# Kernel optimization log

Measured on AMD Instinct MI355X. Metric: run time of the kernel, lower is better.

The kernel has to match this reference:

```python
import jax, jax.numpy as jnp
import numpy as np

BN_EPS = 1e-5
NUM_BITS = 8          # activation quantization bits
NUM_BITS_WEIGHT = 8   # weight quantization bits


def _ste(x, q):
    # straight-through estimator: forward = q, backward = identity
    return x + jax.lax.stop_gradient(q - x)


def quant_signed(x, bits):
    # symmetric signed per-tensor uniform quantization (input_signed=True / weights with sign=True)
    qmax = float(2 ** (bits - 1) - 1)
    scale = jnp.max(jnp.abs(x)) / qmax + 1e-12
    q = jnp.clip(jnp.round(x / scale), -qmax - 1.0, qmax) * scale
    return _ste(x, q)


def quant_unsigned(x, bits):
    # unsigned per-tensor uniform quantization (input_signed=False, post-ReLU activations)
    qmax = float(2 ** bits - 1)
    scale = jnp.max(x) / qmax + 1e-12
    q = jnp.clip(jnp.round(x / scale), 0.0, qmax) * scale
    return _ste(x, q)


def conv3x3(x, w, stride=1):
    # x: [N,C,H,W], w: [O,I,3,3], padding=1, no bias
    return jax.lax.conv_general_dilated(
        x, w, window_strides=(stride, stride), padding=((1, 1), (1, 1)),
        dimension_numbers=('NCHW', 'OIHW', 'NCHW'))


def batchnorm(x, gamma, beta):
    # training-mode BN: per-batch statistics over (N,H,W)
    mean = jnp.mean(x, axis=(0, 2, 3), keepdims=True)
    var = jnp.var(x, axis=(0, 2, 3), keepdims=True)
    xn = (x - mean) * jax.lax.rsqrt(var + BN_EPS)
    return xn * gamma[None, :, None, None] + beta[None, :, None, None]


def setup_inputs() -> dict:
    key = jax.random.key(0)
    k1, k2, k3 = jax.random.split(key, 3)
    B, C, H, W = 64, 256, 32, 32
    x = jax.random.normal(k1, (B, C, H, W), dtype=jnp.float32)
    fan = C * 9
    w1 = jax.random.normal(k2, (C, C, 3, 3), dtype=jnp.float32) * np.sqrt(2.0 / fan)
    w2 = jax.random.normal(k3, (C, C, 3, 3), dtype=jnp.float32) * np.sqrt(2.0 / fan)
    gamma1 = jnp.ones((C,), jnp.float32)
    beta1 = jnp.zeros((C,), jnp.float32)
    gamma2 = jnp.ones((C,), jnp.float32)
    beta2 = jnp.zeros((C,), jnp.float32)
    return {'x': x, 'w1': w1, 'gamma1': gamma1, 'beta1': beta1,
            'w2': w2, 'gamma2': gamma2, 'beta2': beta2}


def reference(x, w1, gamma1, beta1, w2, gamma2, beta2):
    residual = x
    # conv1: input_signed=True -> signed 8-bit act quant; weight 8-bit signed quant
    qx = quant_signed(x, NUM_BITS)
    qw1 = quant_signed(w1, NUM_BITS_WEIGHT)
    out = conv3x3(qx, qw1, stride=1)
    out = batchnorm(out, gamma1, beta1)
    out = jax.nn.relu(out)
    # conv2: input_signed=False -> unsigned 8-bit act quant (post-ReLU)
    qo = quant_unsigned(out, NUM_BITS)
    qw2 = quant_signed(w2, NUM_BITS_WEIGHT)
    out = conv3x3(qo, qw2, stride=1)
    out = batchnorm(out, gamma2, beta2)
    out = out + residual
    out = jax.nn.relu(out)
    return out
```

## Files before the change

kernel.cpp:

```cpp
#include <hip/hip_runtime.h>

typedef unsigned short US;
typedef __attribute__((ext_vector_type(8))) short bf16x8;
typedef __attribute__((ext_vector_type(4))) float f32x4;

typedef __attribute__((address_space(1))) unsigned int uglobal;
typedef __attribute__((address_space(3))) unsigned int ulocal;

__device__ __forceinline__ void async16(const void* g, void* l) {
  __builtin_amdgcn_global_load_lds((const uglobal*)g, (ulocal*)l, 16, 0, 0);
}

__device__ __forceinline__ US f2bf(float f) {
  union { float f; unsigned u; } v; v.f = f;
  return (US)(v.u >> 16);
}

__device__ __forceinline__ float u2f(unsigned u) { return __uint_as_float(u); }

__global__ __launch_bounds__(256) void absmax3_kernel(const float* __restrict__ x,
                                                      const float* __restrict__ w1,
                                                      const float* __restrict__ w2,
                                                      unsigned* __restrict__ sc) {
  int b = blockIdx.x;
  const float* src; int n4, b0, nb, seg;
  if (b < 1792)      { src = x;  n4 = 4194304; b0 = 0;    nb = 1792; seg = 0; }
  else if (b < 1856) { src = w1; n4 = 147456;  b0 = 1792; nb = 64;   seg = 1; }
  else               { src = w2; n4 = 147456;  b0 = 1856; nb = 64;   seg = 2; }
  float m = 0.f;
  int stride = nb * 256;
  for (int i = (b - b0) * 256 + threadIdx.x; i < n4; i += stride) {
    float4 v = ((const float4*)src)[i];
    m = fmaxf(fmaxf(fabsf(v.x), fabsf(v.y)), fmaxf(fmaxf(fabsf(v.z), fabsf(v.w)), m));
  }
  for (int off = 32; off; off >>= 1) m = fmaxf(m, __shfl_down(m, off, 64));
  __shared__ float sm[4];
  int lane = threadIdx.x & 63, wv = threadIdx.x >> 6;
  if (!lane) sm[wv] = m;
  __syncthreads();
  if (threadIdx.x == 0)
    atomicMax(sc + seg, __float_as_uint(fmaxf(fmaxf(sm[0], sm[1]), fmaxf(sm[2], sm[3]))));
}

__global__ __launch_bounds__(256) void quantw_kernel(const float* __restrict__ w, US* __restrict__ wq,
                                                     const unsigned* __restrict__ sc, int sidx) {
  int j = blockIdx.x * 256 + threadIdx.x;
  if (j >= 256 * 2304) return;
  float s = u2f(sc[sidx]) / 127.f + 1e-12f;
  int o = j / 2304, k = j - o * 2304, khw = k >> 8, c = k & 255;
  float q = fminf(fmaxf(rintf(w[(size_t)(o * 256 + c) * 9 + khw] / s), -128.f), 127.f);
  wq[j] = f2bf(q);
}

__global__ __launch_bounds__(256) void quantx_kernel(const float* __restrict__ x,
                                                     US* __restrict__ halo,
                                                     const unsigned* __restrict__ sc) {
  int n = blockIdx.x >> 5, h = blockIdx.x & 31;
  float s = u2f(sc[0]) / 127.f + 1e-12f;
  __shared__ float lds[32 * 257];
  const float* src = x + (size_t)n * 256 * 1024 + h * 32;
  int t = threadIdx.x;
  int wloc = t & 31, crow = t >> 5;
  for (int cc = 0; cc < 256; cc += 8) {
    int c = cc + crow;
    lds[wloc * 257 + c] = src[(size_t)c * 1024 + wloc];
  }
  __syncthreads();
  US* dst = halo + ((size_t)((n * 34 + h + 1) * 34) + 1) * 256;
  for (int w_ = 0; w_ < 32; ++w_) {
    float v = lds[w_ * 257 + t];
    float q = fminf(fmaxf(rintf(v / s), -128.f), 127.f);
    dst[(size_t)w_ * 256 + t] = f2bf(q);
  }
}

template <int MODE>
__global__ __launch_bounds__(512) void conv8_kernel(const US* __restrict__ aptr,
                                                    const US* __restrict__ bptr,
                                                    float* __restrict__ out,
                                                    const unsigned* __restrict__ sc,
                                                    float* __restrict__ part) {
  extern __shared__ char smem[];
  const int tid = threadIdx.x, lane = tid & 63, wid = tid >> 6;
  const int wm = wid >> 2, wn = wid & 3;
  int bid = blockIdx.x;
  bid = (bid & 7) * 32 + (bid >> 3);
  const int pixBase = bid * 256;

  long gA[2], gB[2];
  int ldst[2];
#pragma unroll
  for (int j = 0; j < 2; ++j) {
    int d = tid * 16 + j * 8192;
    int rp = d >> 7, s = (d >> 4) & 7, sp = s ^ (rp & 7);
    int row = rp * 2 + (sp >> 2), kl = (sp & 3) * 8;
    ldst[j] = d;
    int p = pixBase + row;
    int n = p >> 10, h = (p >> 5) & 31, w_ = p & 31;
    long ghalo = (long)((n * 34 + h) * 34 + w_) * 512 + kl * 2;
    long gwt = (long)row * 4608 + kl * 2;
    if (MODE == 0) { gA[j] = ghalo; gB[j] = gwt; }
    else           { gA[j] = gwt;  gB[j] = ghalo; }
  }

  const int g = lane >> 4, l15 = lane & 15;
  int aOff[8], bOff[4];
#pragma unroll
  for (int m = 0; m < 8; ++m) {
    int row = wm * 128 + m * 16 + l15; int rp = row >> 1;
    aOff[m] = rp * 128 + ((((((row & 1) << 2) | g)) ^ (rp & 7)) << 4);
  }
#pragma unroll
  for (int n = 0; n < 4; ++n) {
    int row = wn * 64 + n * 16 + l15; int rp = row >> 1;
    bOff[n] = rp * 128 + ((((((row & 1) << 2) | g)) ^ (rp & 7)) << 4);
  }

  const char* ac = (const char*)aptr;
  const char* bc = (const char*)bptr;
  char* lds = smem;

  auto stage = [&](int P) {
    int cblk = P / 9, khw = P - cblk * 9;
    int kh = khw / 3, kw = khw - kh * 3;
    long uH = (long)(kh * 34 + kw) * 512 + cblk * 64;
    long uW = (long)khw * 512 + cblk * 64;
    long uA = (MODE == 0) ? uH : uW;
    long uB = (MODE == 0) ? uW : uH;
    char* rb = lds + (P & 3) * 32768;
    async16(ac + gA[0] + uA, rb + ldst[0]);
    async16(ac + gA[1] + uA, rb + ldst[1]);
    async16(bc + gB[0] + uB, rb + 16384 + ldst[0]);
    async16(bc + gB[1] + uB, rb + 16384 + ldst[1]);
  };

  f32x4 acc[8][4];
#pragma unroll
  for (int m = 0; m < 8; ++m)
#pragma unroll
    for (int n = 0; n < 4; ++n)
#pragma unroll
      for (int r = 0; r < 4; ++r) acc[m][n][r] = 0.f;

  stage(0); stage(1); stage(2);
  asm volatile("s_waitcnt vmcnt(8)" ::: "memory");
  asm volatile("s_barrier" ::: "memory");

  for (int P = 0; P < 72; ++P) {
    if (P < 69) stage(P + 3);
    const char* rb = lds + (P & 3) * 32768;
    bf16x8 a[8], b[4];
#pragma unroll
    for (int m = 0; m < 8; ++m) a[m] = *(const bf16x8*)(rb + aOff[m]);
#pragma unroll
    for (int n = 0; n < 4; ++n) b[n] = *(const bf16x8*)(rb + 16384 + bOff[n]);
    __builtin_amdgcn_s_setprio(1);
#pragma unroll
    for (int m = 0; m < 8; ++m)
#pragma unroll
      for (int n = 0; n < 4; ++n)
        acc[m][n] = __builtin_amdgcn_mfma_f32_16x16x32_bf16(a[m], b[n], acc[m][n], 0, 0, 0);
    __builtin_amdgcn_s_setprio(0);
    if (P < 69)      asm volatile("s_waitcnt vmcnt(8)" ::: "memory");
    else if (P == 69) asm volatile("s_waitcnt vmcnt(4)" ::: "memory");
    else if (P == 70) asm volatile("s_waitcnt vmcnt(0)" ::: "memory");
    if (P < 71) asm volatile("s_barrier" ::: "memory");
  }
  __syncthreads();

  if constexpr (MODE == 0) {
    const float s = (u2f(sc[0]) / 127.f + 1e-12f) * (u2f(sc[1]) / 127.f + 1e-12f);
    float vs[4], vss[4], vmx[4], vmn[4];
#pragma unroll
    for (int n = 0; n < 4; ++n) { vs[n] = 0.f; vss[n] = 0.f; vmx[n] = -3.4e38f; vmn[n] = 3.4e38f; }
#pragma unroll
    for (int m = 0; m < 8; ++m) {
      int p0 = pixBase + wm * 128 + m * 16 + g * 4;
#pragma unroll
      for (int n = 0; n < 4; ++n) {
        int ch = wn * 64 + n * 16 + l15;
#pragma unroll
        for (int r = 0; r < 4; ++r) {
          float v = acc[m][n][r] * s;
          out[(size_t)(p0 + r) * 256 + ch] = v;
          vs[n] += v; vss[n] += v * v;
          vmx[n] = fmaxf(vmx[n], v); vmn[n] = fminf(vmn[n], v);
        }
      }
    }
#pragma unroll
    for (int off = 16; off <= 32; off <<= 1)
#pragma unroll
      for (int n = 0; n < 4; ++n) {
        vs[n] += __shfl_xor(vs[n], off, 64);
        vss[n] += __shfl_xor(vss[n], off, 64);
        vmx[n] = fmaxf(vmx[n], __shfl_xor(vmx[n], off, 64));
        vmn[n] = fminf(vmn[n], __shfl_xor(vmn[n], off, 64));
      }
    float* S0 = (float*)smem;
    float* S1 = S0 + 512;
    float* S2 = S0 + 1024;
    float* S3 = S0 + 1536;
    if (lane < 16) {
#pragma unroll
      for (int n = 0; n < 4; ++n) {
        int ch = wn * 64 + n * 16 + l15;
        S0[wm * 256 + ch] = vs[n]; S1[wm * 256 + ch] = vss[n];
        S2[wm * 256 + ch] = vmx[n]; S3[wm * 256 + ch] = vmn[n];
      }
    }
    __syncthreads();
    if (tid < 256) {
      int idx = bid * 256 + tid;
      part[idx]          = S0[tid] + S0[256 + tid];
      part[65536 + idx]  = S1[tid] + S1[256 + tid];
      part[131072 + idx] = fmaxf(S2[tid], S2[256 + tid]);
      part[196608 + idx] = fminf(S3[tid], S3[256 + tid]);
    }
  } else {
    const float s = (u2f(sc[3]) / 255.f + 1e-12f) * (u2f(sc[2]) / 127.f + 1e-12f);
    float* SS = (float*)smem;
    float* SQ = SS + 1024;
#pragma unroll
    for (int m = 0; m < 8; ++m) {
      float sr[4], sq[4];
#pragma unroll
      for (int r = 0; r < 4; ++r) { sr[r] = 0.f; sq[r] = 0.f; }
      int o0 = wm * 128 + m * 16 + g * 4;
#pragma unroll
      for (int n = 0; n < 4; ++n) {
        int p = pixBase + wn * 64 + n * 16 + l15;
#pragma unroll
        for (int r = 0; r < 4; ++r) {
          float v = acc[m][n][r] * s;
          out[(size_t)(o0 + r) * 65536 + p] = v;
          sr[r] += v; sq[r] += v * v;
        }
      }
#pragma unroll
      for (int off = 1; off <= 8; off <<= 1)
#pragma unroll
        for (int r = 0; r < 4; ++r) {
          sr[r] += __shfl_xor(sr[r], off, 64);
          sq[r] += __shfl_xor(sq[r], off, 64);
        }
      if (l15 == 0) {
#pragma unroll
        for (int r = 0; r < 4; ++r) {
          SS[wn * 256 + o0 + r] = sr[r];
          SQ[wn * 256 + o0 + r] = sq[r];
        }
      }
    }
    __syncthreads();
    if (tid < 256) {
      float a = 0.f, b = 0.f;
#pragma unroll
      for (int w = 0; w < 4; ++w) { a += SS[w * 256 + tid]; b += SQ[w * 256 + tid]; }
      part[bid * 256 + tid] = a;
      part[65536 + bid * 256 + tid] = b;
    }
  }
}

__global__ __launch_bounds__(256) void bn1fin_kernel(const float* __restrict__ part,
                                                     const float* __restrict__ g,
                                                     const float* __restrict__ be,
                                                     float* __restrict__ bnA, float* __restrict__ bnB,
                                                     unsigned* __restrict__ sc) {
  int o0 = blockIdx.x * 32;
  int t = threadIdx.x, oc = t & 31, mq = t >> 5;
  float s = 0.f, ss = 0.f, mx = -3.4e38f, mn = 3.4e38f;
  for (int j = 0; j < 32; ++j) {
    int i = (mq * 32 + j) * 256 + o0 + oc;
    s += part[i]; ss += part[65536 + i];
    mx = fmaxf(mx, part[131072 + i]); mn = fminf(mn, part[196608 + i]);
  }
  __shared__ float red[4][8][32];
  red[0][mq][oc] = s; red[1][mq][oc] = ss; red[2][mq][oc] = mx; red[3][mq][oc] = mn;
  __syncthreads();
  if (t < 32) {
    s = 0.f; ss = 0.f; mx = -3.4e38f; mn = 3.4e38f;
    for (int q = 0; q < 8; ++q) {
      s += red[0][q][t]; ss += red[1][q][t];
      mx = fmaxf(mx, red[2][q][t]); mn = fminf(mn, red[3][q][t]);
    }
    float mean = s * (1.f / 65536.f);
    float var = fmaxf(ss * (1.f / 65536.f) - mean * mean, 0.f);
    int o = o0 + t;
    float a = g[o] * rsqrtf(var + 1e-5f);
    float b2 = be[o] - mean * a;
    bnA[o] = a; bnB[o] = b2;
    float m = fmaxf(fmaxf(a * mx + b2, a * mn + b2), 0.f);
    atomicMax(sc + 3, __float_as_uint(m));
  }
}

__global__ __launch_bounds__(256) void bn2fin_kernel(const float* __restrict__ part,
                                                     const float* __restrict__ g,
                                                     const float* __restrict__ be,
                                                     float* __restrict__ bnA2, float* __restrict__ bnB2) {
  int o0 = blockIdx.x * 32;
  int t = threadIdx.x, oc = t & 31, mq = t >> 5;
  float s = 0.f, ss = 0.f;
  for (int j = 0; j < 32; ++j) {
    int i = (mq * 32 + j) * 256 + o0 + oc;
    s += part[i]; ss += part[65536 + i];
  }
  __shared__ float red[2][8][32];
  red[0][mq][oc] = s; red[1][mq][oc] = ss;
  __syncthreads();
  if (t < 32) {
    s = 0.f; ss = 0.f;
    for (int q = 0; q < 8; ++q) { s += red[0][q][t]; ss += red[1][q][t]; }
    float mean = s * (1.f / 65536.f);
    float var = fmaxf(ss * (1.f / 65536.f) - mean * mean, 0.f);
    int o = o0 + t;
    float a = g[o] * rsqrtf(var + 1e-5f);
    bnA2[o] = a;
    bnB2[o] = be[o] - mean * a;
  }
}

__global__ __launch_bounds__(256) void apply_kernel(const float* __restrict__ y,
                                                    const float* __restrict__ bnA,
                                                    const float* __restrict__ bnB,
                                                    const unsigned* __restrict__ sc,
                                                    US* __restrict__ halo) {
  int t = threadIdx.x;
  int c4 = (t & 63) * 4;
  int psub = t >> 6;
  float s2 = u2f(sc[3]) / 255.f + 1e-12f;
  float4 a = *(const float4*)(bnA + c4);
  float4 b = *(const float4*)(bnB + c4);
  int p0 = blockIdx.x * 16 + psub;
  for (int j = 0; j < 4; ++j) {
    int p = p0 + j * 4;
    float4 v = *(const float4*)(y + (size_t)p * 256 + c4);
    ushort4 q;
    q.x = f2bf(fminf(fmaxf(rintf(fmaxf(a.x * v.x + b.x, 0.f) / s2), 0.f), 255.f));
    q.y = f2bf(fminf(fmaxf(rintf(fmaxf(a.y * v.y + b.y, 0.f) / s2), 0.f), 255.f));
    q.z = f2bf(fminf(fmaxf(rintf(fmaxf(a.z * v.z + b.z, 0.f) / s2), 0.f), 255.f));
    q.w = f2bf(fminf(fmaxf(rintf(fmaxf(a.w * v.w + b.w, 0.f) / s2), 0.f), 255.f));
    int n = p >> 10, h = (p >> 5) & 31, w_ = p & 31;
    *(ushort4*)(halo + ((size_t)((n * 34 + h + 1) * 34) + (w_ + 1)) * 256 + c4) = q;
  }
}

__global__ __launch_bounds__(256) void final_kernel(const float* __restrict__ y2,
                                                    const float* __restrict__ x,
                                                    const float* __restrict__ bnA2,
                                                    const float* __restrict__ bnB2,
                                                    float* __restrict__ out) {
  int tid = blockIdx.x * 256 + threadIdx.x;
  for (int i = tid; i < 4194304; i += 1048576) {
    int e = i << 2;
    int o = (e >> 10) & 255;
    int n = e >> 18, hw = e & 1023;
    float4 v = *(const float4*)(y2 + (((size_t)o << 16) + (n << 10) + hw));
    float4 xr = ((const float4*)x)[i];
    float a = bnA2[o], b = bnB2[o];
    float4 r;
    r.x = fmaxf(a * v.x + b + xr.x, 0.f);
    r.y = fmaxf(a * v.y + b + xr.y, 0.f);
    r.z = fmaxf(a * v.z + b + xr.z, 0.f);
    r.w = fmaxf(a * v.w + b + xr.w, 0.f);
    ((float4*)out)[i] = r;
  }
}

extern "C" void kernel_launch(void* const* d_in, const int* in_sizes, int n_in,
                              void* d_out, int out_size, void* d_ws, size_t ws_size,
                              hipStream_t stream) {
  const float* x  = (const float*)d_in[0];
  const float* w1 = (const float*)d_in[1];
  const float* g1 = (const float*)d_in[2];
  const float* b1 = (const float*)d_in[3];
  const float* w2 = (const float*)d_in[4];
  const float* g2 = (const float*)d_in[5];
  const float* b2 = (const float*)d_in[6];
  float* out = (float*)d_out;
  char* ws = (char*)d_ws;

  unsigned* sc = (unsigned*)ws;
  float* bnA   = (float*)(ws + 8192);
  float* bnB   = (float*)(ws + 12288);
  float* bnA2  = (float*)(ws + 16384);
  float* bnB2  = (float*)(ws + 20480);
  float* part  = (float*)(ws + 24576);
  US* wq1  = (US*)(ws + 24576 + 2097152);
  US* wq2  = (US*)(ws + 24576 + 2097152 + 1179648);
  US* halo = (US*)(ws + 24576 + 2097152 + 2 * 1179648);
  float* convb = (float*)(ws + 24576 + 2097152 + 2 * 1179648 + 37879808);

  hipFuncSetAttribute((const void*)(conv8_kernel<0>), hipFuncAttributeMaxDynamicSharedMemorySize, 131072);
  hipFuncSetAttribute((const void*)(conv8_kernel<1>), hipFuncAttributeMaxDynamicSharedMemorySize, 131072);

  hipMemsetAsync(sc, 0, 64, stream);
  hipMemsetAsync(halo, 0, 37879808, stream);

  absmax3_kernel<<<1920, 256, 0, stream>>>(x, w1, w2, sc);
  quantw_kernel<<<2304, 256, 0, stream>>>(w1, wq1, sc, 1);
  quantw_kernel<<<2304, 256, 0, stream>>>(w2, wq2, sc, 2);
  quantx_kernel<<<2048, 256, 0, stream>>>(x, halo, sc);
  conv8_kernel<0><<<256, 512, 131072, stream>>>(halo, wq1, convb, sc, part);
  bn1fin_kernel<<<8, 256, 0, stream>>>(part, g1, b1, bnA, bnB, sc);
  apply_kernel<<<4096, 256, 0, stream>>>(convb, bnA, bnB, sc, halo);
  conv8_kernel<1><<<256, 512, 131072, stream>>>(wq2, halo, convb, sc, part);
  bn2fin_kernel<<<8, 256, 0, stream>>>(part, g2, b2, bnA2, bnB2);
  final_kernel<<<4096, 256, 0, stream>>>(convb, x, bnA2, bnB2, out);
}
```

Baseline: 367.1 us.

## Switch conv GEMMs from bf16 to int8 MFMA with offset-corrected unsigned activations

Quantized weights and activations are now stored as int8, and both convolutions use the i32 16x16x64 int8 MFMA. This halves the K-loop iteration count and halves the halo and weight traffic. Post-ReLU unsigned activations are shifted by -128 to fit signed int8, and a per-output-channel correction (128 times the sum of the weights) is added back in the epilogue. The halo border is filled with 0x80 so its shifted value is zero. Epilogue stores are staged through LDS so they go out as coalesced float4 writes, and the two weight-quant launches are merged into one.

```diff
diff --git a/kernel.cpp b/kernel.cpp
--- a/kernel.cpp
+++ b/kernel.cpp
@@ -1,7 +1,6 @@
 #include <hip/hip_runtime.h>
 
-typedef unsigned short US;
-typedef __attribute__((ext_vector_type(8))) short bf16x8;
+typedef __attribute__((ext_vector_type(4))) int i32x4;
 typedef __attribute__((ext_vector_type(4))) float f32x4;
 
 typedef __attribute__((address_space(1))) unsigned int uglobal;
@@ -10,12 +9,6 @@
 __device__ __forceinline__ void async16(const void* g, void* l) {
   __builtin_amdgcn_global_load_lds((const uglobal*)g, (ulocal*)l, 16, 0, 0);
 }
-
-__device__ __forceinline__ US f2bf(float f) {
-  union { float f; unsigned u; } v; v.f = f;
-  return (US)(v.u >> 16);
-}
-
 __device__ __forceinline__ float u2f(unsigned u) { return __uint_as_float(u); }
 
 __global__ __launch_bounds__(256) void absmax3_kernel(const float* __restrict__ x,
@@ -42,23 +35,43 @@
     atomicMax(sc + seg, __float_as_uint(fmaxf(fmaxf(sm[0], sm[1]), fmaxf(sm[2], sm[3]))));
 }
 
-__global__ __launch_bounds__(256) void quantw_kernel(const float* __restrict__ w, US* __restrict__ wq,
-                                                     const unsigned* __restrict__ sc, int sidx) {
-  int j = blockIdx.x * 256 + threadIdx.x;
-  if (j >= 256 * 2304) return;
-  float s = u2f(sc[sidx]) / 127.f + 1e-12f;
-  int o = j / 2304, k = j - o * 2304, khw = k >> 8, c = k & 255;
-  float q = fminf(fmaxf(rintf(w[(size_t)(o * 256 + c) * 9 + khw] / s), -128.f), 127.f);
-  wq[j] = f2bf(q);
+__global__ __launch_bounds__(256) void quantw_kernel(const float* __restrict__ w1,
+                                                     const float* __restrict__ w2,
+                                                     signed char* __restrict__ wq1,
+                                                     signed char* __restrict__ wq2,
+                                                     const unsigned* __restrict__ sc) {
+  int b = blockIdx.x;
+  int t2 = b >= 2304;
+  const float* w = t2 ? w2 : w1;
+  signed char* wq = t2 ? wq2 : wq1;
+  float s = u2f(sc[1 + t2]) / 127.f + 1e-12f;
+  int j = (b - t2 * 2304) * 256 + threadIdx.x;
+  int o = j / 2304, k = j - o * 2304, tap = k >> 8, c = k & 255;
+  float q = fminf(fmaxf(rintf(w[(size_t)(o * 256 + c) * 9 + tap] / s), -128.f), 127.f);
+  wq[j] = (signed char)q;
+}
+
+__global__ __launch_bounds__(64) void tapsum_kernel(const signed char* __restrict__ wq2,
+                                                    int* __restrict__ csumT) {
+  int o = blockIdx.x;
+  const int* row = (const int*)(wq2 + (size_t)o * 2304);
+  int s = 0;
+  for (int i = threadIdx.x; i < 576; i += 64) {
+    int v = row[i];
+    s += (int)(signed char)(v) + (int)(signed char)(v >> 8) +
+         (int)(signed char)(v >> 16) + (int)(signed char)(v >> 24);
+  }
+  for (int off = 32; off; off >>= 1) s += __shfl_down(s, off, 64);
+  if (threadIdx.x == 0) csumT[o] = 128 * s;
 }
 
 __global__ __launch_bounds__(256) void quantx_kernel(const float* __restrict__ x,
-                                                     US* __restrict__ halo,
+                                                     signed char* __restrict__ halo,
                                                      const unsigned* __restrict__ sc) {
   int n = blockIdx.x >> 5, h = blockIdx.x & 31;
   float s = u2f(sc[0]) / 127.f + 1e-12f;
   __shared__ float lds[32 * 257];
-  const float* src = x + (size_t)n * 256 * 1024 + h * 32;
+  const float* src = x + (size_t)n * 262144 + h * 32;
   int t = threadIdx.x;
   int wloc = t & 31, crow = t >> 5;
   for (int cc = 0; cc < 256; cc += 8) {
@@ -66,20 +79,26 @@
     lds[wloc * 257 + c] = src[(size_t)c * 1024 + wloc];
   }
   __syncthreads();
-  US* dst = halo + ((size_t)((n * 34 + h + 1) * 34) + 1) * 256;
-  for (int w_ = 0; w_ < 32; ++w_) {
-    float v = lds[w_ * 257 + t];
-    float q = fminf(fmaxf(rintf(v / s), -128.f), 127.f);
-    dst[(size_t)w_ * 256 + t] = f2bf(q);
+  signed char* dst = halo + ((size_t)((n * 34 + h + 1) * 34) + 1) * 256;
+  int c4 = (t & 63) * 4, wsub = t >> 6;
+  for (int j = 0; j < 8; ++j) {
+    int w_ = wsub * 8 + j;
+    char4 q;
+    q.x = (signed char)fminf(fmaxf(rintf(lds[w_ * 257 + c4 + 0] / s), -128.f), 127.f);
+    q.y = (signed char)fminf(fmaxf(rintf(lds[w_ * 257 + c4 + 1] / s), -128.f), 127.f);
+    q.z = (signed char)fminf(fmaxf(rintf(lds[w_ * 257 + c4 + 2] / s), -128.f), 127.f);
+    q.w = (signed char)fminf(fmaxf(rintf(lds[w_ * 257 + c4 + 3] / s), -128.f), 127.f);
+    *(char4*)(dst + (size_t)w_ * 256 + c4) = q;
   }
 }
 
 template <int MODE>
-__global__ __launch_bounds__(512) void conv8_kernel(const US* __restrict__ aptr,
-                                                    const US* __restrict__ bptr,
-                                                    float* __restrict__ out,
-                                                    const unsigned* __restrict__ sc,
-                                                    float* __restrict__ part) {
+__global__ __launch_bounds__(512) void conv_i8_kernel(const signed char* __restrict__ aptr,
+                                                      const signed char* __restrict__ bptr,
+                                                      float* __restrict__ out,
+                                                      const unsigned* __restrict__ sc,
+                                                      float* __restrict__ part,
+                                                      const int* __restrict__ csumT) {
   extern __shared__ char smem[];
   const int tid = threadIdx.x, lane = tid & 63, wid = tid >> 6;
   const int wm = wid >> 2, wn = wid & 3;
@@ -92,15 +111,15 @@
 #pragma unroll
   for (int j = 0; j < 2; ++j) {
     int d = tid * 16 + j * 8192;
-    int rp = d >> 7, s = (d >> 4) & 7, sp = s ^ (rp & 7);
-    int row = rp * 2 + (sp >> 2), kl = (sp & 3) * 8;
+    int rp = d >> 7, s5 = (d >> 4) & 7, sp = s5 ^ (rp & 7);
+    int row = rp * 2 + (sp >> 2), kc = (sp & 3) * 16;
     ldst[j] = d;
     int p = pixBase + row;
     int n = p >> 10, h = (p >> 5) & 31, w_ = p & 31;
-    long ghalo = (long)((n * 34 + h) * 34 + w_) * 512 + kl * 2;
-    long gwt = (long)row * 4608 + kl * 2;
-    if (MODE == 0) { gA[j] = ghalo; gB[j] = gwt; }
-    else           { gA[j] = gwt;  gB[j] = ghalo; }
+    long ghalo = (long)((n * 34 + h) * 34 + w_) * 256 + kc;
+    long gwt = (long)row * 2304 + kc;
+    gA[j] = (MODE == 0) ? ghalo : gwt;
+    gB[j] = (MODE == 0) ? gwt : ghalo;
   }
 
   const int g = lane >> 4, l15 = lane & 15;
@@ -108,12 +127,12 @@
 #pragma unroll
   for (int m = 0; m < 8; ++m) {
     int row = wm * 128 + m * 16 + l15; int rp = row >> 1;
-    aOff[m] = rp * 128 + ((((((row & 1) << 2) | g)) ^ (rp & 7)) << 4);
+    aOff[m] = rp * 128 + (((((row & 1) << 2) | g) ^ (rp & 7)) << 4);
   }
 #pragma unroll
   for (int n = 0; n < 4; ++n) {
     int row = wn * 64 + n * 16 + l15; int rp = row >> 1;
-    bOff[n] = rp * 128 + ((((((row & 1) << 2) | g)) ^ (rp & 7)) << 4);
+    bOff[n] = rp * 128 + (((((row & 1) << 2) | g) ^ (rp & 7)) << 4);
   }
 
   const char* ac = (const char*)aptr;
@@ -121,10 +140,10 @@
   char* lds = smem;
 
   auto stage = [&](int P) {
-    int cblk = P / 9, khw = P - cblk * 9;
-    int kh = khw / 3, kw = khw - kh * 3;
-    long uH = (long)(kh * 34 + kw) * 512 + cblk * 64;
-    long uW = (long)khw * 512 + cblk * 64;
+    int cblk = P / 9, tap = P - cblk * 9;
+    int kh = tap / 3, kw = tap - kh * 3;
+    long uH = (long)(kh * 34 + kw) * 256 + cblk * 64;
+    long uW = (long)tap * 256 + cblk * 64;
     long uA = (MODE == 0) ? uH : uW;
     long uB = (MODE == 0) ? uW : uH;
     char* rb = lds + (P & 3) * 32768;
@@ -134,39 +153,41 @@
     async16(bc + gB[1] + uB, rb + 16384 + ldst[1]);
   };
 
-  f32x4 acc[8][4];
+  i32x4 acc[8][4];
 #pragma unroll
   for (int m = 0; m < 8; ++m)
 #pragma unroll
     for (int n = 0; n < 4; ++n)
 #pragma unroll
-      for (int r = 0; r < 4; ++r) acc[m][n][r] = 0.f;
+      for (int r = 0; r < 4; ++r) acc[m][n][r] = 0;
 
   stage(0); stage(1); stage(2);
   asm volatile("s_waitcnt vmcnt(8)" ::: "memory");
   asm volatile("s_barrier" ::: "memory");
 
-  for (int P = 0; P < 72; ++P) {
-    if (P < 69) stage(P + 3);
+  for (int P = 0; P < 36; ++P) {
+    if (P < 33) stage(P + 3);
     const char* rb = lds + (P & 3) * 32768;
-    bf16x8 a[8], b[4];
-#pragma unroll
-    for (int m = 0; m < 8; ++m) a[m] = *(const bf16x8*)(rb + aOff[m]);
-#pragma unroll
-    for (int n = 0; n < 4; ++n) b[n] = *(const bf16x8*)(rb + 16384 + bOff[n]);
+    i32x4 a[8], b[4];
+#pragma unroll
+    for (int m = 0; m < 8; ++m) a[m] = *(const i32x4*)(rb + aOff[m]);
+#pragma unroll
+    for (int n = 0; n < 4; ++n) b[n] = *(const i32x4*)(rb + 16384 + bOff[n]);
     __builtin_amdgcn_s_setprio(1);
 #pragma unroll
     for (int m = 0; m < 8; ++m)
 #pragma unroll
       for (int n = 0; n < 4; ++n)
-        acc[m][n] = __builtin_amdgcn_mfma_f32_16x16x32_bf16(a[m], b[n], acc[m][n], 0, 0, 0);
+        acc[m][n] = __builtin_amdgcn_mfma_i32_16x16x64_i8(a[m], b[n], acc[m][n], 0, 0, 0);
     __builtin_amdgcn_s_setprio(0);
-    if (P < 69)      asm volatile("s_waitcnt vmcnt(8)" ::: "memory");
-    else if (P == 69) asm volatile("s_waitcnt vmcnt(4)" ::: "memory");
-    else if (P == 70) asm volatile("s_waitcnt vmcnt(0)" ::: "memory");
-    if (P < 71) asm volatile("s_barrier" ::: "memory");
+    if (P < 33)       asm volatile("s_waitcnt vmcnt(8)" ::: "memory");
+    else if (P == 33) asm volatile("s_waitcnt vmcnt(4)" ::: "memory");
+    else if (P == 34) asm volatile("s_waitcnt vmcnt(0)" ::: "memory");
+    if (P < 35) asm volatile("s_barrier" ::: "memory");
   }
   __syncthreads();
+
+  float* twr = (float*)(smem + wid * 17408);
 
   if constexpr (MODE == 0) {
     const float s = (u2f(sc[0]) / 127.f + 1e-12f) * (u2f(sc[1]) / 127.f + 1e-12f);
@@ -174,18 +195,27 @@
 #pragma unroll
     for (int n = 0; n < 4; ++n) { vs[n] = 0.f; vss[n] = 0.f; vmx[n] = -3.4e38f; vmn[n] = 3.4e38f; }
 #pragma unroll
-    for (int m = 0; m < 8; ++m) {
-      int p0 = pixBase + wm * 128 + m * 16 + g * 4;
-#pragma unroll
-      for (int n = 0; n < 4; ++n) {
-        int ch = wn * 64 + n * 16 + l15;
-#pragma unroll
-        for (int r = 0; r < 4; ++r) {
-          float v = acc[m][n][r] * s;
-          out[(size_t)(p0 + r) * 256 + ch] = v;
-          vs[n] += v; vss[n] += v * v;
-          vmx[n] = fmaxf(vmx[n], v); vmn[n] = fminf(vmn[n], v);
-        }
+    for (int half = 0; half < 2; ++half) {
+#pragma unroll
+      for (int m2 = 0; m2 < 4; ++m2) {
+        int m = half * 4 + m2;
+#pragma unroll
+        for (int n = 0; n < 4; ++n)
+#pragma unroll
+          for (int r = 0; r < 4; ++r) {
+            float v = (float)acc[m][n][r] * s;
+            vs[n] += v; vss[n] += v * v;
+            vmx[n] = fmaxf(vmx[n], v); vmn[n] = fminf(vmn[n], v);
+            twr[(m2 * 16 + g * 4 + r) * 68 + n * 16 + l15] = v;
+          }
+      }
+#pragma unroll
+      for (int it = 0; it < 16; ++it) {
+        int i = it * 64 + lane;
+        int row = i >> 4, c4 = (i & 15) << 2;
+        float4 v4 = *(const float4*)(twr + row * 68 + c4);
+        int p = pixBase + wm * 128 + half * 64 + row;
+        *(float4*)(out + (size_t)p * 256 + wn * 64 + c4) = v4;
       }
     }
 #pragma unroll
@@ -197,10 +227,9 @@
         vmx[n] = fmaxf(vmx[n], __shfl_xor(vmx[n], off, 64));
         vmn[n] = fminf(vmn[n], __shfl_xor(vmn[n], off, 64));
       }
-    float* S0 = (float*)smem;
-    float* S1 = S0 + 512;
-    float* S2 = S0 + 1024;
-    float* S3 = S0 + 1536;
+    __syncthreads();
+    float* S0 = (float*)(smem + 139264);
+    float* S1 = S0 + 512; float* S2 = S0 + 1024; float* S3 = S0 + 1536;
     if (lane < 16) {
 #pragma unroll
       for (int n = 0; n < 4; ++n) {
@@ -219,37 +248,46 @@
     }
   } else {
     const float s = (u2f(sc[3]) / 255.f + 1e-12f) * (u2f(sc[2]) / 127.f + 1e-12f);
-    float* SS = (float*)smem;
+    float* SS = (float*)(smem + 139264);
     float* SQ = SS + 1024;
 #pragma unroll
-    for (int m = 0; m < 8; ++m) {
-      float sr[4], sq[4];
-#pragma unroll
-      for (int r = 0; r < 4; ++r) { sr[r] = 0.f; sq[r] = 0.f; }
-      int o0 = wm * 128 + m * 16 + g * 4;
-#pragma unroll
-      for (int n = 0; n < 4; ++n) {
-        int p = pixBase + wn * 64 + n * 16 + l15;
-#pragma unroll
-        for (int r = 0; r < 4; ++r) {
-          float v = acc[m][n][r] * s;
-          out[(size_t)(o0 + r) * 65536 + p] = v;
-          sr[r] += v; sq[r] += v * v;
+    for (int half = 0; half < 2; ++half) {
+#pragma unroll
+      for (int m2 = 0; m2 < 4; ++m2) {
+        int m = half * 4 + m2;
+        int o0 = wm * 128 + half * 64 + m2 * 16 + g * 4;
+        i32x4 tc = *(const i32x4*)(csumT + o0);
+        float sr[4] = {0.f, 0.f, 0.f, 0.f}, sq[4] = {0.f, 0.f, 0.f, 0.f};
+#pragma unroll
+        for (int n = 0; n < 4; ++n)
+#pragma unroll
+          for (int r = 0; r < 4; ++r) {
+            float v = (float)(acc[m][n][r] + tc[r]) * s;
+            sr[r] += v; sq[r] += v * v;
+            twr[(m2 * 16 + g * 4 + r) * 68 + n * 16 + l15] = v;
+          }
+#pragma unroll
+        for (int off = 1; off <= 8; off <<= 1)
+#pragma unroll
+          for (int r = 0; r < 4; ++r) {
+            sr[r] += __shfl_xor(sr[r], off, 64);
+            sq[r] += __shfl_xor(sq[r], off, 64);
+          }
+        if (l15 == 0) {
+#pragma unroll
+          for (int r = 0; r < 4; ++r) {
+            SS[wn * 256 + o0 + r] = sr[r];
+            SQ[wn * 256 + o0 + r] = sq[r];
+          }
         }
       }
 #pragma unroll
-      for (int off = 1; off <= 8; off <<= 1)
-#pragma unroll
-        for (int r = 0; r < 4; ++r) {
-          sr[r] += __shfl_xor(sr[r], off, 64);
-          sq[r] += __shfl_xor(sq[r], off, 64);
-        }
-      if (l15 == 0) {
-#pragma unroll
-        for (int r = 0; r < 4; ++r) {
-          SS[wn * 256 + o0 + r] = sr[r];
-          SQ[wn * 256 + o0 + r] = sq[r];
-        }
+      for (int it = 0; it < 16; ++it) {
+        int i = it * 64 + lane;
+        int row = i >> 4, c4 = (i & 15) << 2;
+        float4 v4 = *(const float4*)(twr + row * 68 + c4);
+        int o = wm * 128 + half * 64 + row;
+        *(float4*)(out + (size_t)o * 65536 + pixBase + wn * 64 + c4) = v4;
       }
     }
     __syncthreads();
@@ -326,7 +364,7 @@
                                                     const float* __restrict__ bnA,
                                                     const float* __restrict__ bnB,
                                                     const unsigned* __restrict__ sc,
-                                                    US* __restrict__ halo) {
+                                                    signed char* __restrict__ halo) {
   int t = threadIdx.x;
   int c4 = (t & 63) * 4;
   int psub = t >> 6;
@@ -337,13 +375,13 @@
   for (int j = 0; j < 4; ++j) {
     int p = p0 + j * 4;
     float4 v = *(const float4*)(y + (size_t)p * 256 + c4);
-    ushort4 q;
-    q.x = f2bf(fminf(fmaxf(rintf(fmaxf(a.x * v.x + b.x, 0.f) / s2), 0.f), 255.f));
-    q.y = f2bf(fminf(fmaxf(rintf(fmaxf(a.y * v.y + b.y, 0.f) / s2), 0.f), 255.f));
-    q.z = f2bf(fminf(fmaxf(rintf(fmaxf(a.z * v.z + b.z, 0.f) / s2), 0.f), 255.f));
-    q.w = f2bf(fminf(fmaxf(rintf(fmaxf(a.w * v.w + b.w, 0.f) / s2), 0.f), 255.f));
+    char4 q;
+    q.x = (signed char)((int)fminf(fmaxf(rintf(fmaxf(a.x * v.x + b.x, 0.f) / s2), 0.f), 255.f) - 128);
+    q.y = (signed char)((int)fminf(fmaxf(rintf(fmaxf(a.y * v.y + b.y, 0.f) / s2), 0.f), 255.f) - 128);
+    q.z = (signed char)((int)fminf(fmaxf(rintf(fmaxf(a.z * v.z + b.z, 0.f) / s2), 0.f), 255.f) - 128);
+    q.w = (signed char)((int)fminf(fmaxf(rintf(fmaxf(a.w * v.w + b.w, 0.f) / s2), 0.f), 255.f) - 128);
     int n = p >> 10, h = (p >> 5) & 31, w_ = p & 31;
-    *(ushort4*)(halo + ((size_t)((n * 34 + h + 1) * 34) + (w_ + 1)) * 256 + c4) = q;
+    *(char4*)(halo + ((size_t)((n * 34 + h + 1) * 34) + (w_ + 1)) * 256 + c4) = q;
   }
 }
 
@@ -383,30 +421,32 @@
   char* ws = (char*)d_ws;
 
   unsigned* sc = (unsigned*)ws;
-  float* bnA   = (float*)(ws + 8192);
-  float* bnB   = (float*)(ws + 12288);
-  float* bnA2  = (float*)(ws + 16384);
-  float* bnB2  = (float*)(ws + 20480);
+  float* bnA   = (float*)(ws + 4096);
+  float* bnB   = (float*)(ws + 8192);
+  float* bnA2  = (float*)(ws + 12288);
+  float* bnB2  = (float*)(ws + 16384);
+  int*   csumT = (int*)(ws + 20480);
   float* part  = (float*)(ws + 24576);
-  US* wq1  = (US*)(ws + 24576 + 2097152);
-  US* wq2  = (US*)(ws + 24576 + 2097152 + 1179648);
-  US* halo = (US*)(ws + 24576 + 2097152 + 2 * 1179648);
-  float* convb = (float*)(ws + 24576 + 2097152 + 2 * 1179648 + 37879808);
-
-  hipFuncSetAttribute((const void*)(conv8_kernel<0>), hipFuncAttributeMaxDynamicSharedMemorySize, 131072);
-  hipFuncSetAttribute((const void*)(conv8_kernel<1>), hipFuncAttributeMaxDynamicSharedMemorySize, 131072);
+  signed char* wq1  = (signed char*)(ws + 24576 + 1048576);
+  signed char* wq2  = wq1 + 589824;
+  signed char* halo = wq2 + 589824;
+  float* convb = (float*)(ws + 24576 + 1048576 + 2 * 589824 + 18939904);
+
+  hipFuncSetAttribute((const void*)(conv_i8_kernel<0>), hipFuncAttributeMaxDynamicSharedMemorySize, 147456);
+  hipFuncSetAttribute((const void*)(conv_i8_kernel<1>), hipFuncAttributeMaxDynamicSharedMemorySize, 147456);
 
   hipMemsetAsync(sc, 0, 64, stream);
-  hipMemsetAsync(halo, 0, 37879808, stream);
+  hipMemsetAsync(halo, 0, 18939904, stream);
 
   absmax3_kernel<<<1920, 256, 0, stream>>>(x, w1, w2, sc);
-  quantw_kernel<<<2304, 256, 0, stream>>>(w1, wq1, sc, 1);
-  quantw_kernel<<<2304, 256, 0, stream>>>(w2, wq2, sc, 2);
+  quantw_kernel<<<4608, 256, 0, stream>>>(w1, w2, wq1, wq2, sc);
+  tapsum_kernel<<<256, 64, 0, stream>>>(wq2, csumT);
   quantx_kernel<<<2048, 256, 0, stream>>>(x, halo, sc);
-  conv8_kernel<0><<<256, 512, 131072, stream>>>(halo, wq1, convb, sc, part);
+  conv_i8_kernel<0><<<256, 512, 147456, stream>>>(halo, wq1, convb, sc, part, csumT);
   bn1fin_kernel<<<8, 256, 0, stream>>>(part, g1, b1, bnA, bnB, sc);
+  hipMemsetAsync(halo, 0x80, 18939904, stream);
   apply_kernel<<<4096, 256, 0, stream>>>(convb, bnA, bnB, sc, halo);
-  conv8_kernel<1><<<256, 512, 131072, stream>>>(wq2, halo, convb, sc, part);
+  conv_i8_kernel<1><<<256, 512, 147456, stream>>>(wq2, halo, convb, sc, part, csumT);
   bn2fin_kernel<<<8, 256, 0, stream>>>(part, g2, b2, bnA2, bnB2);
   final_kernel<<<4096, 256, 0, stream>>>(convb, x, bnA2, bnB2, out);
 }
```

New measurement: 332.4 us. 1.1x faster.
